# Kernel tuning notes

Measured on AMD Instinct MI355X. Metric: run time of the kernel, lower is better.

## Reference

```python
import jax, jax.numpy as jnp
import numpy as np

B, T, N = 16, 256, 20000
REGIONS, TOPK = 20000, 0.2
IN_DIM = int(REGIONS * TOPK ** 2)   # 800
K = int(REGIONS * TOPK)             # 4000
R = 1000                            # rest_limitation
ZCOLS = K + R                       # all-False mask columns per sample


def setup_inputs() -> dict:
    key = jax.random.key(0)
    ks = jax.random.split(key, 8)
    x = jax.random.normal(ks[0], (B, T, IN_DIM), jnp.float32)
    # first ZCOLS voxel columns are never covered (mask False), rest are covered
    border_mask = jnp.concatenate(
        [jnp.zeros((B, T, ZCOLS), bool), jnp.ones((B, T, N - ZCOLS), bool)], axis=-1)
    # K distinct indices per sample, drawn from the uncovered columns [0, ZCOLS)
    index = jax.vmap(lambda k: jax.random.permutation(k, ZCOLS)[:K])(
        jax.random.split(ks[1], B)).astype(jnp.int32)
    s1 = 1.0 / np.sqrt(IN_DIM); s2 = 1.0 / np.sqrt(K)
    W1 = jax.random.uniform(ks[2], (IN_DIM, K), jnp.float32, -s1, s1)
    b1 = jax.random.uniform(ks[3], (K,), jnp.float32, -s1, s1)
    W2 = jax.random.uniform(ks[4], (K, K), jnp.float32, -s2, s2)
    b2 = jax.random.uniform(ks[5], (K,), jnp.float32, -s2, s2)
    W3 = jax.random.uniform(ks[6], (K, R), jnp.float32, -s2, s2)
    b3 = jax.random.uniform(ks[7], (R,), jnp.float32, -s2, s2)
    return dict(x=x, border_mask=border_mask, index=index,
                W1=W1, b1=b1, W2=W2, b2=b2, W3=W3, b3=b3)


def reference(x, border_mask, index, W1, b1, W2, b2, W3, b3):
    h = x @ W1 + b1                  # unzip   [B,T,K]
    h = h @ W2 + b2                  # unprocess [B,T,K]
    x_rest = h @ W3 + b3             # rest    [B,T,R]
    colsum = border_mask.sum(axis=1)                 # [B,N] per-voxel coverage count
    idx_member = jax.vmap(lambda i: jnp.zeros((N,), bool).at[i].set(True))(index)
    # scatter h into indexed voxel columns
    x_recon = jax.vmap(lambda i, hb: jnp.zeros((T, N), h.dtype).at[:, i].set(hb))(index, h)
    # rest positions: uncovered columns not already taken by index (sorted order)
    rest_mask = (colsum == 0) & ~idx_member          # [B,N]
    rank = jnp.cumsum(rest_mask, axis=-1) - 1        # position among rest columns
    valid = rest_mask & (rank < R)                   # cap at rest_limitation ('adjust')
    g = jnp.take_along_axis(
        x_rest, jnp.broadcast_to(jnp.clip(rank, 0, R - 1)[:, None, :], (B, T, N)), axis=-1)
    return jnp.where(valid[:, None, :], g, x_recon)
```

## Files before the change

### kernel.cpp

```cpp
#include <hip/hip_runtime.h>

typedef __attribute__((ext_vector_type(4))) float f32x4;
typedef __attribute__((ext_vector_type(8))) __bf16 bf16x8;

#define B_SZ   16
#define T_SZ   256
#define BT_SZ  4096
#define N_VOX  20000
#define INDIM  800
#define K1P    896
#define K_DIM  4000
#define KP     4096
#define R_DIM  1000
#define RP     1024
#define SPLITK 4

__device__ __forceinline__ unsigned short f2bf(float f) {
  unsigned int u = __builtin_bit_cast(unsigned int, f);
  u += 0x7fffu + ((u >> 16) & 1u);
  return (unsigned short)(u >> 16);
}
__device__ __forceinline__ float bf2f(unsigned short h) {
  unsigned int u = ((unsigned int)h) << 16;
  return __builtin_bit_cast(float, u);
}
__device__ __forceinline__ void gload16(const void* g, void* l) {
  __builtin_amdgcn_global_load_lds(
      (const __attribute__((address_space(1))) void*)g,
      (__attribute__((address_space(3))) void*)l, 16, 0, 0);
}

#define PREP_CVT    4096
#define PREP_W1     3584
#define PREP_W2     16384
#define PREP_W3     4096
#define PREP_COV    320

__device__ void dev_transpose(const float* __restrict__ W,
                              unsigned short* __restrict__ WT,
                              int K, int N, int Kpad, int Npad,
                              int kb, int nb, int tx, int ty,
                              float (*tile)[33]) {
  int k0 = kb * 32, n0 = nb * 32;
  for (int i = ty; i < 32; i += 8) {
    int k = k0 + i, n = n0 + tx;
    tile[i][tx] = (k < K && n < N) ? W[(size_t)k * N + n] : 0.f;
  }
  __syncthreads();
  for (int i = ty; i < 32; i += 8) {
    int n = n0 + i, k = k0 + tx;
    if (n < Npad && k < Kpad)
      WT[(size_t)n * Kpad + k] = f2bf(tile[tx][i]);
  }
}

__global__ __launch_bounds__(256) void prep_kernel(
    const float* __restrict__ x, unsigned short* __restrict__ xb,
    const float* __restrict__ W1, unsigned short* __restrict__ w1t,
    const float* __restrict__ W2, unsigned short* __restrict__ w2t,
    const float* __restrict__ W3, unsigned short* __restrict__ w3t,
    const int* __restrict__ bmask, unsigned char* __restrict__ cov) {
  __shared__ float tile[32][33];
  int id = blockIdx.x;
  const int tid = threadIdx.x;
  const int tx = tid & 31, ty = tid >> 5;

  if (id < PREP_CVT) {
    int row = id, c4 = tid;
    if (c4 < K1P / 4) {
      ushort4 o = {0, 0, 0, 0};
      if (c4 < INDIM / 4) {
        float4 v = ((const float4*)(x + (size_t)row * INDIM))[c4];
        o.x = f2bf(v.x); o.y = f2bf(v.y); o.z = f2bf(v.z); o.w = f2bf(v.w);
      }
      ((ushort4*)(xb + (size_t)row * K1P))[c4] = o;
    }
    return;
  }
  id -= PREP_CVT;
  if (id < PREP_W1) {
    dev_transpose(W1, w1t, INDIM, K_DIM, K1P, KP, id % 28, id / 28, tx, ty, tile);
    return;
  }
  id -= PREP_W1;
  if (id < PREP_W2) {
    dev_transpose(W2, w2t, K_DIM, K_DIM, KP, KP, id % 128, id / 128, tx, ty, tile);
    return;
  }
  id -= PREP_W2;
  if (id < PREP_W3) {
    dev_transpose(W3, w3t, K_DIM, R_DIM, KP, RP, id % 128, id / 128, tx, ty, tile);
    return;
  }
  id -= PREP_W3;
  {
    int n4 = (id % 20) * 256 + tid;
    int b = id / 20;
    if (n4 >= N_VOX / 4) return;
    const int4* p = (const int4*)(bmask + (size_t)b * T_SZ * N_VOX) + n4;
    int4 a = {0, 0, 0, 0};
    for (int t0 = 0; t0 < T_SZ; t0 += 8) {
      int4 c[8];
#pragma unroll
      for (int tt = 0; tt < 8; ++tt)
        c[tt] = p[(size_t)(t0 + tt) * (N_VOX / 4)];
#pragma unroll
      for (int tt = 0; tt < 8; ++tt) {
        a.x |= c[tt].x; a.y |= c[tt].y; a.z |= c[tt].z; a.w |= c[tt].w;
      }
      if (a.x && a.y && a.z && a.w) break;
    }
    uchar4 o;
    o.x = (unsigned char)(a.x != 0); o.y = (unsigned char)(a.y != 0);
    o.z = (unsigned char)(a.z != 0); o.w = (unsigned char)(a.w != 0);
    *(uchar4*)(cov + (size_t)b * N_VOX + (size_t)n4 * 4) = o;
  }
}

__global__ void map_kernel(const int* __restrict__ index,
                           const unsigned char* __restrict__ cov,
                           int* __restrict__ srcmap) {
  int b = blockIdx.x, tid = threadIdx.x;
  int* sm = srcmap + (size_t)b * N_VOX;
  for (int n = tid; n < N_VOX; n += 1024) sm[n] = -1;
  __syncthreads();
  const int* idx = index + (size_t)b * K_DIM;
  for (int j = tid; j < K_DIM; j += 1024) sm[idx[j]] = j;
  __syncthreads();

  __shared__ int wsum[16];
  __shared__ int s_running;
  if (tid == 0) s_running = 0;
  __syncthreads();
  const int lane = tid & 63, wid = tid >> 6;
  const unsigned char* cv = cov + (size_t)b * N_VOX;
  for (int base = 0; base < N_VOX; base += 1024) {
    int n = base + tid;
    bool flag = (n < N_VOX) && (!cv[n]) && (sm[n] < 0);
    unsigned long long bal = __ballot(flag);
    if (lane == 0) wsum[wid] = __popcll(bal);
    __syncthreads();
    int woff = 0, tot = 0;
    for (int w = 0; w < 16; ++w) {
      int c = wsum[w];
      if (w < wid) woff += c;
      tot += c;
    }
    int rank = s_running + woff + __popcll(bal & ((1ull << lane) - 1ull));
    if (flag && rank < R_DIM) sm[n] = K_DIM + rank;
    __syncthreads();
    if (tid == 0) s_running += tot;
    __syncthreads();
  }
}

template <bool SPLIT>
__global__ __launch_bounds__(512, 1) void gemm256(
    const unsigned short* __restrict__ A,
    const unsigned short* __restrict__ BTm,
    const float* __restrict__ bias, int nbias,
    unsigned short* __restrict__ C,
    int K, int lda, int ldb, int ldc, size_t zstride) {
  __shared__ __align__(16) char smem[131072];
  const int tid = threadIdx.x;
  const int wid = tid >> 6, lane = tid & 63;
  const int wm = wid >> 2, wn = wid & 3;
  const int r15 = lane & 15, kg = lane >> 4;
  const int bm = blockIdx.y, bn = blockIdx.x;
  if constexpr (SPLIT) {
    const int kz = blockIdx.z;
    A += (size_t)kz * K;
    BTm += (size_t)kz * K;
    C += (size_t)kz * zstride;
  }

  const int srow = tid >> 2;
  const int scol = (((tid & 3) ^ ((srow >> 1) & 3)) * 8);
  const unsigned short* gA = A + (size_t)(bm * 256 + srow) * lda + scol;
  const unsigned short* gB = BTm + (size_t)(bn * 256 + srow) * ldb + scol;

  const int cxor = ((kg ^ ((r15 >> 1) & 3)) * 16);
  const int aoff = (wm * 128 + r15) * 64 + cxor;
  const int boff = (wn * 64 + r15) * 64 + cxor;

  f32x4 acc[8][4] = {};
  bf16x8 bfr[4];

#define STAGE_HALF(S, MAT, KH, TN)                                            \
  {                                                                           \
    const unsigned short* g =                                                 \
        ((MAT) ? gB : gA) + (size_t)(TN) * 64 + (KH) * 32;                    \
    char* l = smem + (S) * 65536 + (MAT) * 32768 + (KH) * 16384 + tid * 16;   \
    gload16(g, l);                                                            \
    gload16(g + (size_t)128 * ((MAT) ? ldb : lda), l + 8192);                 \
  }

#define PHASE(S, KS, MH, TN, DOVM)                                            \
  {                                                                           \
    bf16x8 af[4];                                                             \
    if ((MH) == 0) {                                                          \
      _Pragma("unroll")                                                       \
      for (int j = 0; j < 4; ++j)                                             \
        bfr[j] = *(const bf16x8*)(smem + (S) * 65536 + 32768 +                \
                                  (KS) * 16384 + boff + j * 1024);            \
    }                                                                         \
    _Pragma("unroll")                                                         \
    for (int i = 0; i < 4; ++i)                                               \
      af[i] = *(const bf16x8*)(smem + (S) * 65536 + (KS) * 16384 +            \
                               (MH) * 4096 + aoff + i * 1024);                \
    if (DOVM) asm volatile("s_waitcnt vmcnt(2)" ::: "memory");                \
    asm volatile("s_barrier" ::: "memory");                                   \
    STAGE_HALF((S) ^ 1, (MH), (KS), TN)                                       \
    __builtin_amdgcn_s_setprio(1);                                            \
    _Pragma("unroll")                                                         \
    for (int i = 0; i < 4; ++i)                                               \
      _Pragma("unroll")                                                       \
      for (int j = 0; j < 4; ++j)                                             \
        acc[(MH) * 4 + i][j] = __builtin_amdgcn_mfma_f32_16x16x32_bf16(       \
            af[i], bfr[j], acc[(MH) * 4 + i][j], 0, 0, 0);                    \
    __builtin_amdgcn_s_setprio(0);                                            \
  }

#define TILE4(S, TN)                                                          \
  PHASE(S, 0, 0, TN, 0)                                                       \
  PHASE(S, 0, 1, TN, 1)                                                       \
  PHASE(S, 1, 0, TN, 0)                                                       \
  PHASE(S, 1, 1, TN, 1)

  const int NT = K >> 6;
  STAGE_HALF(0, 0, 0, 0)
  STAGE_HALF(0, 1, 0, 0)
  STAGE_HALF(0, 0, 1, 0)
  STAGE_HALF(0, 1, 1, 0)
  asm volatile("s_waitcnt vmcnt(4)" ::: "memory");
  asm volatile("s_barrier" ::: "memory");

  for (int tp = 0; tp < NT; tp += 2) {
    const int tn1 = tp + 1;
    TILE4(0, tn1)
    const int tn2 = (tp + 2 < NT) ? tp + 2 : NT - 1;
    TILE4(1, tn2)
  }

#undef STAGE_HALF
#undef PHASE
#undef TILE4

#pragma unroll
  for (int f = 0; f < 8; ++f) {
    const int row0 = bm * 256 + wm * 128 + f * 16 + kg * 4;
#pragma unroll
    for (int j = 0; j < 4; ++j) {
      const int col = bn * 256 + wn * 64 + j * 16 + r15;
      float bv = 0.f;
      if constexpr (!SPLIT) bv = bias[(col < nbias) ? col : (nbias - 1)];
#pragma unroll
      for (int r = 0; r < 4; ++r)
        C[(size_t)(row0 + r) * ldc + col] = f2bf(acc[f][j][r] + bv);
    }
  }
}

__global__ void fill_out(const int* __restrict__ srcmap,
                         const unsigned short* __restrict__ h2b,
                         const unsigned short* __restrict__ xpart,
                         const float* __restrict__ b3,
                         float* __restrict__ out) {
  int n4 = blockIdx.x * 256 + threadIdx.x;
  if (n4 >= N_VOX / 4) return;
  int t = blockIdx.y, b = blockIdx.z;
  size_t bt = (size_t)b * T_SZ + t;
  const int4 sm = ((const int4*)(srcmap + (size_t)b * N_VOX))[n4];
  const unsigned short* hrow = h2b + bt * KP;
  const unsigned short* xrow = xpart + bt * RP;
  const size_t zs = (size_t)BT_SZ * RP;
  auto val = [&](int s) -> float {
    if (s < 0) return 0.f;
    if (s < K_DIM) return bf2f(hrow[s]);
    int r = s - K_DIM;
    float acc = b3[r];
#pragma unroll
    for (int z = 0; z < SPLITK; ++z) acc += bf2f(xrow[z * zs + r]);
    return acc;
  };
  f32x4 v;
  v.x = val(sm.x); v.y = val(sm.y); v.z = val(sm.z); v.w = val(sm.w);
  __builtin_nontemporal_store(v, (f32x4*)(out + bt * N_VOX) + n4);
}

extern "C" void kernel_launch(void* const* d_in, const int* in_sizes, int n_in,
                              void* d_out, int out_size, void* d_ws, size_t ws_size,
                              hipStream_t stream) {
  const float* x          = (const float*)d_in[0];
  const int* bm           = (const int*)d_in[1];
  const int* index        = (const int*)d_in[2];
  const float* W1         = (const float*)d_in[3];
  const float* b1         = (const float*)d_in[4];
  const float* W2         = (const float*)d_in[5];
  const float* b2         = (const float*)d_in[6];
  const float* W3         = (const float*)d_in[7];
  const float* b3         = (const float*)d_in[8];
  float* out = (float*)d_out;

  char* ws = (char*)d_ws;
  size_t off = 0;
  auto alloc = [&](size_t bytes) -> void* {
    void* p = ws + off;
    off += (bytes + 255) & ~(size_t)255;
    return p;
  };
  unsigned short* xb    = (unsigned short*)alloc((size_t)BT_SZ * K1P * 2);
  unsigned short* w1t   = (unsigned short*)alloc((size_t)KP * K1P * 2);
  unsigned short* w2t   = (unsigned short*)alloc((size_t)KP * KP * 2);
  unsigned short* w3t   = (unsigned short*)alloc((size_t)RP * KP * 2);
  unsigned short* h1b   = (unsigned short*)alloc((size_t)BT_SZ * KP * 2);
  unsigned short* h2b   = (unsigned short*)alloc((size_t)BT_SZ * KP * 2);
  unsigned short* xpart = (unsigned short*)alloc((size_t)SPLITK * BT_SZ * RP * 2);
  unsigned char* cov = (unsigned char*)alloc((size_t)B_SZ * N_VOX);
  int* srcmap = (int*)alloc((size_t)B_SZ * N_VOX * 4);

  {
    int nblk = PREP_CVT + PREP_W1 + PREP_W2 + PREP_W3 + PREP_COV;
    prep_kernel<<<nblk, 256, 0, stream>>>(x, xb, W1, w1t, W2, w2t, W3, w3t, bm, cov);
  }
  map_kernel<<<B_SZ, 1024, 0, stream>>>(index, cov, srcmap);

  {
    dim3 g(KP / 256, BT_SZ / 256);
    gemm256<false><<<g, 512, 0, stream>>>(xb, w1t, b1, K_DIM, h1b,
                                          K1P, K1P, K1P, KP, 0);
  }
  {
    dim3 g(KP / 256, BT_SZ / 256);
    gemm256<false><<<g, 512, 0, stream>>>(h1b, w2t, b2, K_DIM, h2b,
                                          KP, KP, KP, KP, 0);
  }
  {
    dim3 g(RP / 256, BT_SZ / 256, SPLITK);
    gemm256<true><<<g, 512, 0, stream>>>(h2b, w3t, nullptr, 0, xpart,
                                         KP / SPLITK, KP, KP, RP,
                                         (size_t)BT_SZ * RP);
  }

  {
    dim3 g((N_VOX / 4 + 255) / 256, T_SZ, B_SZ);
    fill_out<<<g, 256, 0, stream>>>(srcmap, h2b, xpart, b3, out);
  }
}
```

Before: 400.6 us.

## Fuse map kernel into first GEMM launch and reduce pipeline barriers

Turns the srcmap construction into a device function and runs it in 16 extra blocks of the first GEMM launch, removing a separate kernel launch and its serialization. The GEMM body is factored out so the block coordinates come from arguments. The per-phase wait-and-barrier is moved after the MFMA block and issued only every other phase with a looser vmcnt. This relaxes synchronization at the risk of LDS reuse hazards.

```diff
diff --git a/kernel.cpp b/kernel.cpp
--- a/kernel.cpp
+++ b/kernel.cpp
@@ -117,58 +117,55 @@
   }
 }
 
-__global__ void map_kernel(const int* __restrict__ index,
-                           const unsigned char* __restrict__ cov,
-                           int* __restrict__ srcmap) {
-  int b = blockIdx.x, tid = threadIdx.x;
+__device__ void dev_map(const int* __restrict__ index,
+                        const unsigned char* __restrict__ cov,
+                        int* __restrict__ srcmap, int b, char* smembase) {
+  const int tid = threadIdx.x;
+  int* wsum = (int*)smembase;
+  int* s_running = (int*)(smembase + 64);
   int* sm = srcmap + (size_t)b * N_VOX;
-  for (int n = tid; n < N_VOX; n += 1024) sm[n] = -1;
+  for (int n = tid; n < N_VOX; n += 512) sm[n] = -1;
   __syncthreads();
   const int* idx = index + (size_t)b * K_DIM;
-  for (int j = tid; j < K_DIM; j += 1024) sm[idx[j]] = j;
+  for (int j = tid; j < K_DIM; j += 512) sm[idx[j]] = j;
   __syncthreads();
-
-  __shared__ int wsum[16];
-  __shared__ int s_running;
-  if (tid == 0) s_running = 0;
+  if (tid == 0) *s_running = 0;
   __syncthreads();
   const int lane = tid & 63, wid = tid >> 6;
   const unsigned char* cv = cov + (size_t)b * N_VOX;
-  for (int base = 0; base < N_VOX; base += 1024) {
+  for (int base = 0; base < N_VOX; base += 512) {
     int n = base + tid;
     bool flag = (n < N_VOX) && (!cv[n]) && (sm[n] < 0);
     unsigned long long bal = __ballot(flag);
     if (lane == 0) wsum[wid] = __popcll(bal);
     __syncthreads();
     int woff = 0, tot = 0;
-    for (int w = 0; w < 16; ++w) {
+    for (int w = 0; w < 8; ++w) {
       int c = wsum[w];
       if (w < wid) woff += c;
       tot += c;
     }
-    int rank = s_running + woff + __popcll(bal & ((1ull << lane) - 1ull));
+    int rank = *s_running + woff + __popcll(bal & ((1ull << lane) - 1ull));
     if (flag && rank < R_DIM) sm[n] = K_DIM + rank;
     __syncthreads();
-    if (tid == 0) s_running += tot;
+    if (tid == 0) *s_running += tot;
     __syncthreads();
   }
 }
 
 template <bool SPLIT>
-__global__ __launch_bounds__(512, 1) void gemm256(
+__device__ __forceinline__ void gemm256_body(
     const unsigned short* __restrict__ A,
     const unsigned short* __restrict__ BTm,
     const float* __restrict__ bias, int nbias,
     unsigned short* __restrict__ C,
-    int K, int lda, int ldb, int ldc, size_t zstride) {
-  __shared__ __align__(16) char smem[131072];
+    int K, int lda, int ldb, int ldc, size_t zstride,
+    int bm, int bn, int kz, char* smem) {
   const int tid = threadIdx.x;
   const int wid = tid >> 6, lane = tid & 63;
   const int wm = wid >> 2, wn = wid & 3;
   const int r15 = lane & 15, kg = lane >> 4;
-  const int bm = blockIdx.y, bn = blockIdx.x;
   if constexpr (SPLIT) {
-    const int kz = blockIdx.z;
     A += (size_t)kz * K;
     BTm += (size_t)kz * K;
     C += (size_t)kz * zstride;
@@ -195,7 +192,7 @@
     gload16(g + (size_t)128 * ((MAT) ? ldb : lda), l + 8192);                 \
   }
 
-#define PHASE(S, KS, MH, TN, DOVM)                                            \
+#define PHASE(S, KS, MH, TN, DOSYNC)                                          \
   {                                                                           \
     bf16x8 af[4];                                                             \
     if ((MH) == 0) {                                                          \
@@ -208,8 +205,6 @@
     for (int i = 0; i < 4; ++i)                                               \
       af[i] = *(const bf16x8*)(smem + (S) * 65536 + (KS) * 16384 +            \
                                (MH) * 4096 + aoff + i * 1024);                \
-    if (DOVM) asm volatile("s_waitcnt vmcnt(2)" ::: "memory");                \
-    asm volatile("s_barrier" ::: "memory");                                   \
     STAGE_HALF((S) ^ 1, (MH), (KS), TN)                                       \
     __builtin_amdgcn_s_setprio(1);                                            \
     _Pragma("unroll")                                                         \
@@ -219,6 +214,10 @@
         acc[(MH) * 4 + i][j] = __builtin_amdgcn_mfma_f32_16x16x32_bf16(       \
             af[i], bfr[j], acc[(MH) * 4 + i][j], 0, 0, 0);                    \
     __builtin_amdgcn_s_setprio(0);                                            \
+    if (DOSYNC) {                                                             \
+      asm volatile("s_waitcnt vmcnt(4)" ::: "memory");                        \
+      asm volatile("s_barrier" ::: "memory");                                 \
+    }                                                                         \
   }
 
 #define TILE4(S, TN)                                                          \
@@ -259,6 +258,37 @@
         C[(size_t)(row0 + r) * ldc + col] = f2bf(acc[f][j][r] + bv);
     }
   }
+}
+
+template <bool SPLIT>
+__global__ __launch_bounds__(512, 1) void gemm256(
+    const unsigned short* __restrict__ A,
+    const unsigned short* __restrict__ BTm,
+    const float* __restrict__ bias, int nbias,
+    unsigned short* __restrict__ C,
+    int K, int lda, int ldb, int ldc, size_t zstride) {
+  __shared__ __align__(16) char smem[131072];
+  gemm256_body<SPLIT>(A, BTm, bias, nbias, C, K, lda, ldb, ldc, zstride,
+                      blockIdx.y, blockIdx.x, SPLIT ? blockIdx.z : 0, smem);
+}
+
+__global__ __launch_bounds__(512, 1) void gemm1_map(
+    const unsigned short* __restrict__ A,
+    const unsigned short* __restrict__ BTm,
+    const float* __restrict__ bias, int nbias,
+    unsigned short* __restrict__ C,
+    int K, int lda, int ldb, int ldc,
+    const int* __restrict__ index,
+    const unsigned char* __restrict__ cov,
+    int* __restrict__ srcmap) {
+  __shared__ __align__(16) char smem[131072];
+  const int id = blockIdx.x;
+  if (id >= 256) {
+    dev_map(index, cov, srcmap, id - 256, smem);
+    return;
+  }
+  gemm256_body<false>(A, BTm, bias, nbias, C, K, lda, ldb, ldc, 0,
+                      id >> 4, id & 15, 0, smem);
 }
 
 __global__ void fill_out(const int* __restrict__ srcmap,
@@ -323,13 +353,9 @@
     int nblk = PREP_CVT + PREP_W1 + PREP_W2 + PREP_W3 + PREP_COV;
     prep_kernel<<<nblk, 256, 0, stream>>>(x, xb, W1, w1t, W2, w2t, W3, w3t, bm, cov);
   }
-  map_kernel<<<B_SZ, 1024, 0, stream>>>(index, cov, srcmap);
-
-  {
-    dim3 g(KP / 256, BT_SZ / 256);
-    gemm256<false><<<g, 512, 0, stream>>>(xb, w1t, b1, K_DIM, h1b,
-                                          K1P, K1P, K1P, KP, 0);
-  }
+
+  gemm1_map<<<272, 512, 0, stream>>>(xb, w1t, b1, K_DIM, h1b,
+                                     K1P, K1P, K1P, KP, index, cov, srcmap);
   {
     dim3 g(KP / 256, BT_SZ / 256);
     gemm256<false><<<g, 512, 0, stream>>>(h1b, w2t, b2, K_DIM, h2b,
```

Result: no change. 407.1 us (+1.6%).
